# Performance work log

Hardware: AMD Instinct MI355X
Metric: run time of the kernel (lower is better)

The kernel has to match this reference:

```python
import jax, jax.numpy as jnp
import numpy as np

E = 512   # embed_dim
H = 16    # num_heads
D = E // H  # head_dim = 32
L = 2048  # target (query) length
S = 2048  # source (stored pattern) length
N = 4     # batch
LN_EPS = 1e-5


def setup_inputs() -> dict:
    key = jax.random.key(0)
    ks = jax.random.split(key, 8)
    inv_sqrt_e = 1.0 / np.sqrt(E).astype(np.float32)
    return {
        "query": jax.random.normal(ks[0], (L, N, E), jnp.float32),
        "key_in": jax.random.normal(ks[1], (S, N, E), jnp.float32),
        "value": jax.random.normal(ks[2], (S, N, E), jnp.float32),
        "scaling": jax.random.uniform(ks[3], (H,), jnp.float32),  # per-head beta
        "in_proj_weight": jax.random.normal(ks[4], (3 * E, E), jnp.float32) * inv_sqrt_e,
        "in_proj_bias": jnp.zeros((3 * E,), jnp.float32),
        "p_norm_weight": jnp.ones((D,), jnp.float32),
        "p_norm_bias": jnp.zeros((D,), jnp.float32),
        "out_proj_weight": jax.random.normal(ks[5], (E, E), jnp.float32) * inv_sqrt_e,
        "out_proj_bias": jnp.zeros((E,), jnp.float32),
    }


def reference(query, key_in, value, scaling, in_proj_weight, in_proj_bias,
              p_norm_weight, p_norm_bias, out_proj_weight, out_proj_bias):
    Lq, Nb, Ed = query.shape
    Sk = key_in.shape[0]
    # split packed in-projection (torch Linear convention: y = x @ W^T + b)
    wq, wk, wv = jnp.split(in_proj_weight, 3, axis=0)
    bq, bk, bv = jnp.split(in_proj_bias, 3, axis=0)
    q = jnp.einsum('lne,fe->lnf', query, wq) + bq
    k = jnp.einsum('sne,fe->snf', key_in, wk) + bk
    v = jnp.einsum('sne,fe->snf', value, wv) + bv
    # (len, N, H*D) -> (N, H, len, D)
    q = q.reshape(Lq, Nb, H, D).transpose(1, 2, 0, 3)
    k = k.reshape(Sk, Nb, H, D).transpose(1, 2, 0, 3)
    v = v.reshape(Sk, Nb, H, D).transpose(1, 2, 0, 3)

    def pattern_norm(x):
        # affine LayerNorm over the association (head) dimension D
        mu = jnp.mean(x, axis=-1, keepdims=True)
        var = jnp.mean(jnp.square(x - mu), axis=-1, keepdims=True)
        return (x - mu) * jax.lax.rsqrt(var + LN_EPS) * p_norm_weight + p_norm_bias

    k = pattern_norm(k)
    v = pattern_norm(v)

    beta = scaling.reshape(1, H, 1, 1)  # per-head inverse-temperature
    scores = jnp.einsum('nhld,nhsd->nhls', q * beta, k)  # [N,H,L,S]
    attn = jax.nn.softmax(scores, axis=-1)  # single Hopfield update (update_steps_max=0)
    out = jnp.einsum('nhls,nhsd->nhld', attn, v)  # [N,H,L,D]
    out = out.transpose(2, 0, 1, 3).reshape(Lq, Nb, H * D)
    out = jnp.einsum('lnf,of->lno', out, out_proj_weight) + out_proj_bias
    return out  # (L, N, E)
```

## Files before the change

kernel.cpp:

```cpp
#include <hip/hip_runtime.h>
#include <cstdint>

#define LN_EPS 1e-5f

typedef _Float16 f16;
typedef _Float16 half4_t __attribute__((ext_vector_type(4)));
typedef _Float16 half8_t __attribute__((ext_vector_type(8)));
typedef __fp16 fp16v2 __attribute__((ext_vector_type(2)));
typedef float f32x4 __attribute__((ext_vector_type(4)));

__device__ __forceinline__ void gl_lds16(const void* g, void* l) {
    __builtin_amdgcn_global_load_lds(
        (__attribute__((address_space(1))) void*)(uintptr_t)g,
        (__attribute__((address_space(3))) void*)(uint32_t)(uintptr_t)l,
        16, 0, 0);
}

__device__ __forceinline__ half4_t pack4(float a, float b, float c, float d) {
    fp16v2 lo = __builtin_amdgcn_cvt_pkrtz(a, b);
    fp16v2 hi = __builtin_amdgcn_cvt_pkrtz(c, d);
    half4_t r;
    r[0] = (f16)lo[0]; r[1] = (f16)lo[1]; r[2] = (f16)hi[0]; r[3] = (f16)hi[1];
    return r;
}

__global__ void k_cast(const float* __restrict__ W1f, const float* __restrict__ W2f,
                       const float* __restrict__ Xq, const float* __restrict__ Xk,
                       const float* __restrict__ Xv,
                       f16* __restrict__ W1h, f16* __restrict__ W2h,
                       f16* __restrict__ Xh) {
    int t0 = blockIdx.x * blockDim.x + threadIdx.x;
    #pragma unroll
    for (int rep = 0; rep < 4; ++rep) {
        int t = t0 + rep * 851968;
        const float4* src;
        half4_t* dst;
        int idx;
        if (t < 196608)      { src = (const float4*)W1f; dst = (half4_t*)W1h; idx = t; }
        else if (t < 262144) { src = (const float4*)W2f; dst = (half4_t*)W2h; idx = t - 196608; }
        else {
            int u = t - 262144;
            int s = u >> 20;
            idx = u & 1048575;
            src = (s == 0) ? (const float4*)Xq : ((s == 1) ? (const float4*)Xk : (const float4*)Xv);
            dst = (half4_t*)(Xh + (size_t)s * 4194304);
        }
        float4 v = src[idx];
        dst[idx] = pack4(v.x, v.y, v.z, v.w);
    }
}

__global__ __launch_bounds__(256) void k_inproj(
    const f16* __restrict__ Xh, const f16* __restrict__ W1,
    const float* __restrict__ bias, const float* __restrict__ scaling,
    const float* __restrict__ pnw, const float* __restrict__ pnb,
    f16* __restrict__ Qg, f16* __restrict__ Kg, f16* __restrict__ Vtg)
{
    __shared__ __align__(16) char pool[49152];

    const int tid = threadIdx.x;
    const int bid = blockIdx.x;
    const int jj = bid >> 3;
    const int m0 = ((bid & 7) * 8 + (jj & 7)) * 128;
    const int f0 = (jj >> 3) * 128;
    const int sec = f0 >> 9;
    const f16* X = Xh + (size_t)sec * 4194304;
    f16* Ob = (sec == 0) ? Qg : Kg;

    const int wid = tid >> 6, ln = tid & 63, l15 = ln & 15, quad = ln >> 4;
    const int wm = wid >> 1, wn = wid & 1;
    const int srow = ln >> 2, sco = (ln & 3) * 8;

    f32x4 z4 = {0.f, 0.f, 0.f, 0.f};
    f32x4 acc[4][4];
    #pragma unroll
    for (int i = 0; i < 4; ++i)
        #pragma unroll
        for (int j = 0; j < 4; ++j) acc[i][j] = z4;

    auto issue = [&](int kt, int slot) {
        const int k0 = kt * 32;
        f16* As = (f16*)(pool + slot * 16384);
        f16* Bs = (f16*)(pool + slot * 16384 + 8192);
        #pragma unroll
        for (int i = 0; i < 2; ++i) {
            int row = wid * 32 + i * 16 + srow;
            gl_lds16(W1 + (size_t)(f0 + row) * 512 + k0 + sco,
                     Bs + (wid * 32 + i * 16) * 32);
            gl_lds16(X + (size_t)(m0 + row) * 512 + k0 + sco,
                     As + (wid * 32 + i * 16) * 32);
        }
    };
    issue(0, 0);
    issue(1, 1);

    int slot = 0;
    for (int kt = 0; kt < 16; ++kt) {
        if (kt < 15) asm volatile("s_waitcnt vmcnt(4)" ::: "memory");
        else         asm volatile("s_waitcnt vmcnt(0)" ::: "memory");
        __builtin_amdgcn_s_barrier();

        if (kt < 14) {
            int nb = slot + 2; if (nb >= 3) nb -= 3;
            issue(kt + 2, nb);
        }

        const f16* As = (const f16*)(pool + slot * 16384);
        const f16* Bs = (const f16*)(pool + slot * 16384 + 8192);
        half8_t a[4], b[4];
        #pragma unroll
        for (int i = 0; i < 4; ++i)
            a[i] = *(const half8_t*)(As + (wm * 64 + i * 16 + l15) * 32 + quad * 8);
        #pragma unroll
        for (int j = 0; j < 4; ++j)
            b[j] = *(const half8_t*)(Bs + (wn * 64 + j * 16 + l15) * 32 + quad * 8);
        __builtin_amdgcn_s_setprio(1);
        #pragma unroll
        for (int i = 0; i < 4; ++i)
            #pragma unroll
            for (int j = 0; j < 4; ++j)
                acc[i][j] = __builtin_amdgcn_mfma_f32_16x16x32_f16(b[j], a[i], acc[i][j], 0, 0, 0);
        __builtin_amdgcn_s_setprio(0);

        slot = slot + 1; if (slot == 3) slot = 0;
    }

    __syncthreads();
    f16* Ep = (f16*)pool;

    float sA = 0.f, sB = 0.f;
    float4 wA, wB, bA, bB;
    if (sec == 0) {
        int hbase = ((f0 & 511) >> 5) + wn * 2;
        sA = scaling[hbase] * 1.44269504f;
        sB = scaling[hbase + 1] * 1.44269504f;
    } else {
        wA = *(const float4*)(pnw + quad * 4);
        wB = *(const float4*)(pnw + 16 + quad * 4);
        bA = *(const float4*)(pnb + quad * 4);
        bB = *(const float4*)(pnb + 16 + quad * 4);
    }
    float4 bias4[4];
    #pragma unroll
    for (int j = 0; j < 4; ++j)
        bias4[j] = *(const float4*)(bias + f0 + wn * 64 + j * 16 + quad * 4);

    #pragma unroll
    for (int i = 0; i < 4; ++i) {
        float x[4][4];
        #pragma unroll
        for (int j = 0; j < 4; ++j) {
            x[j][0] = acc[i][j][0] + bias4[j].x;
            x[j][1] = acc[i][j][1] + bias4[j].y;
            x[j][2] = acc[i][j][2] + bias4[j].z;
            x[j][3] = acc[i][j][3] + bias4[j].w;
        }
        if (sec == 0) {
            #pragma unroll
            for (int j = 0; j < 4; ++j) {
                float sc = (j < 2) ? sA : sB;
                #pragma unroll
                for (int r = 0; r < 4; ++r) x[j][r] *= sc;
            }
        } else {
            #pragma unroll
            for (int hp = 0; hp < 2; ++hp) {
                float s1 = 0.f, s2 = 0.f;
                #pragma unroll
                for (int jq = 0; jq < 2; ++jq) {
                    int j = hp * 2 + jq;
                    #pragma unroll
                    for (int r = 0; r < 4; ++r) { s1 += x[j][r]; s2 += x[j][r] * x[j][r]; }
                }
                s1 += __shfl_xor(s1, 16); s1 += __shfl_xor(s1, 32);
                s2 += __shfl_xor(s2, 16); s2 += __shfl_xor(s2, 32);
                float mu = s1 * (1.f / 32.f);
                float rs = rsqrtf(s2 * (1.f / 32.f) - mu * mu + LN_EPS);
                #pragma unroll
                for (int jq = 0; jq < 2; ++jq) {
                    int j = hp * 2 + jq;
                    const float4& wv = (j & 1) ? wB : wA;
                    const float4& bv = (j & 1) ? bB : bA;
                    x[j][0] = (x[j][0] - mu) * rs * wv.x + bv.x;
                    x[j][1] = (x[j][1] - mu) * rs * wv.y + bv.y;
                    x[j][2] = (x[j][2] - mu) * rs * wv.z + bv.z;
                    x[j][3] = (x[j][3] - mu) * rs * wv.w + bv.w;
                }
            }
        }
        int mloc = wm * 64 + i * 16 + l15;
        int key = (mloc >> 2) & 7;
        #pragma unroll
        for (int j = 0; j < 4; ++j) {
            int floc0 = wn * 64 + j * 16 + quad * 4;
            *(half4_t*)(Ep + mloc * 128 + (floc0 ^ (key << 3))) =
                pack4(x[j][0], x[j][1], x[j][2], x[j][3]);
        }
    }
    __syncthreads();

    if (sec < 2) {
        int fgrp = (tid >> 6) * 4 + quad;
        int fs = (f0 & 511) + fgrp * 8;
        int hh = fs >> 5, cc = (fs >> 3) & 3;
        #pragma unroll
        for (int it = 0; it < 8; ++it) {
            int nb = it & 3, lblk = it >> 2;
            int L = lblk * 16 + l15;
            int mloc = nb + 4 * L;
            half8_t v = *(const half8_t*)(Ep + mloc * 128 + ((fgrp ^ (L & 7)) << 3));
            int gg = nb * 16 + hh;
            size_t l = (size_t)(m0 >> 2) + L;
            *(half8_t*)(Ob + (size_t)gg * 65536 + (size_t)cc * 16384 + l * 8) = v;
        }
    } else {
        int seg = m0 >> 8;
        int csb = ((m0 >> 7) & 1) * 4;
        int hbase = (f0 & 511) >> 5;
        #pragma unroll
        for (int p = 0; p < 2; ++p) {
            int idx = tid * 2 + p;
            int g16 = idx >> 5, d = idx & 31;
            int nb = g16 >> 2, hhl = g16 & 3;
            int floc = hhl * 32 + d;
            size_t obase = (size_t)((nb * 16 + hbase + hhl) * 32 + seg) * 2048 + d * 64;
            #pragma unroll
            for (int cq = 0; cq < 4; ++cq) {
                half8_t hv;
                #pragma unroll
                for (int es = 0; es < 8; ++es) {
                    int mloc = nb + 4 * (cq * 8 + es);
                    hv[es] = Ep[mloc * 128 + (floc ^ (es << 3))];
                }
                int csx = (csb + cq) ^ (d & 7);
                *(half8_t*)(Vtg + obase + csx * 8) = hv;
            }
        }
    }
}

__global__ __launch_bounds__(256, 4) void k_flash(
    const f16* __restrict__ Qg, const f16* __restrict__ Kg,
    const f16* __restrict__ Vtg, f16* __restrict__ Og)
{
    __shared__ __align__(16) char smem[40960];

    const int tid = threadIdx.x, wid = tid >> 6, ln = tid & 63;
    const int l15 = ln & 15, quad = ln >> 4, l8 = ln & 7;
    char* Pw = smem + 24576 + wid * 4096;
    const int g = blockIdx.x, h = g & 15, n = g >> 4;
    const int q0 = blockIdx.y * 128;

    half8_t aq[2];
    #pragma unroll
    for (int i = 0; i < 2; ++i)
        aq[i] = *(const half8_t*)(Qg + (size_t)g * 65536 + (size_t)quad * 16384 +
                                  (size_t)(q0 + wid * 32 + i * 16 + l15) * 8);

    const f16* kp = Kg + (size_t)g * 65536 + (size_t)wid * 16384;
    const f16* vp = Vtg + (size_t)(g * 32) * 2048 + wid * 512;
    gl_lds16(kp + (size_t)ln * 8, smem + wid * 1024);
    gl_lds16(vp + (size_t)ln * 8, smem + 12288 + wid * 1024);
    gl_lds16(kp + 512 + (size_t)ln * 8, smem + 4096 + wid * 1024);
    gl_lds16(vp + 2048 + (size_t)ln * 8, smem + 12288 + 4096 + wid * 1024);
    kp += 1024;
    vp += 4096;

    half8_t onesf;
    {
        f16 o = (l15 == 0) ? (f16)1.0f : (f16)0.0f;
        #pragma unroll
        for (int j = 0; j < 8; ++j) onesf[j] = o;
    }

    f32x4 z4 = {0.f, 0.f, 0.f, 0.f};
    f32x4 accO[2][2], accSum[2];
    accO[0][0] = z4; accO[0][1] = z4; accO[1][0] = z4; accO[1][1] = z4;
    accSum[0] = z4; accSum[1] = z4;
    float m_i[2] = {-1e30f, -1e30f};

    const char* K0s = smem;          const char* V0s = smem + 12288;
    const char* K1s = smem + 4096;   const char* V1s = smem + 16384;
    const char* K2s = smem + 8192;   const char* V2s = smem + 20480;

    auto body = [&](const char* Kl, const char* Vt, char* Kn, char* Vn, int st) {
        if (st < 31) asm volatile("s_waitcnt vmcnt(2)" ::: "memory");
        else         asm volatile("s_waitcnt vmcnt(0)" ::: "memory");
        __builtin_amdgcn_s_barrier();

        if (st < 30) {
            gl_lds16(kp + (size_t)ln * 8, Kn + wid * 1024);
            gl_lds16(vp + (size_t)ln * 8, Vn + wid * 1024);
            kp += 512;
            vp += 2048;
        }

        half8_t ak[4];
        #pragma unroll
        for (int mt = 0; mt < 4; ++mt)
            ak[mt] = *(const half8_t*)(Kl + quad * 1024 + (mt * 16 + l15) * 16);
        f32x4 accS[2][4];
        __builtin_amdgcn_s_setprio(1);
        #pragma unroll
        for (int i = 0; i < 2; ++i)
            #pragma unroll
            for (int mt = 0; mt < 4; ++mt)
                accS[i][mt] = __builtin_amdgcn_mfma_f32_16x16x32_f16(ak[mt], aq[i], z4, 0, 0, 0);
        __builtin_amdgcn_s_setprio(0);

        float mn[2];
        bool up = false;
        #pragma unroll
        for (int i = 0; i < 2; ++i) {
            float xm = fmaxf(fmaxf(accS[i][0][0], accS[i][0][1]), accS[i][0][2]);
            xm = fmaxf(fmaxf(xm, accS[i][0][3]), accS[i][1][0]);
            xm = fmaxf(fmaxf(xm, accS[i][1][1]), accS[i][1][2]);
            xm = fmaxf(fmaxf(xm, accS[i][1][3]), accS[i][2][0]);
            xm = fmaxf(fmaxf(xm, accS[i][2][1]), accS[i][2][2]);
            xm = fmaxf(fmaxf(xm, accS[i][2][3]), accS[i][3][0]);
            xm = fmaxf(fmaxf(xm, accS[i][3][1]), accS[i][3][2]);
            xm = fmaxf(xm, accS[i][3][3]);
            xm = fmaxf(xm, __shfl_xor(xm, 16));
            xm = fmaxf(xm, __shfl_xor(xm, 32));
            up = up || (xm > m_i[i] + 8.f);
            mn[i] = fmaxf(m_i[i], xm);
        }
        if (__ballot(up)) {
            #pragma unroll
            for (int i = 0; i < 2; ++i) {
                float alpha = __builtin_amdgcn_exp2f(m_i[i] - mn[i]);
                #pragma unroll
                for (int dt = 0; dt < 2; ++dt)
                    #pragma unroll
                    for (int r = 0; r < 4; ++r) accO[i][dt][r] *= alpha;
                #pragma unroll
                for (int r = 0; r < 4; ++r) accSum[i][r] *= alpha;
                m_i[i] = mn[i];
            }
        }

        #pragma unroll
        for (int i = 0; i < 2; ++i) {
            #pragma unroll
            for (int mt = 0; mt < 4; ++mt) {
                float p0 = __builtin_amdgcn_exp2f(accS[i][mt][0] - m_i[i]);
                float p1 = __builtin_amdgcn_exp2f(accS[i][mt][1] - m_i[i]);
                float p2 = __builtin_amdgcn_exp2f(accS[i][mt][2] - m_i[i]);
                float p3 = __builtin_amdgcn_exp2f(accS[i][mt][3] - m_i[i]);
                int ch = (mt * 2 + (quad >> 1)) ^ l8;
                *(half4_t*)(Pw + (i * 16 + l15) * 128 + ch * 16 + (quad & 1) * 8) =
                    pack4(p0, p1, p2, p3);
            }
        }

        #pragma unroll
        for (int kt = 0; kt < 2; ++kt) {
            half8_t av[2], bp[2];
            #pragma unroll
            for (int dt = 0; dt < 2; ++dt) {
                int d = dt * 16 + l15;
                int cp = (kt * 4 + quad) ^ (l15 & 7);
                av[dt] = *(const half8_t*)(Vt + d * 128 + cp * 16);
            }
            #pragma unroll
            for (int i = 0; i < 2; ++i)
                bp[i] = *(const half8_t*)(Pw + (i * 16 + l15) * 128 +
                                          (((kt * 4 + quad) ^ l8) * 16));
            __builtin_amdgcn_s_setprio(1);
            #pragma unroll
            for (int i = 0; i < 2; ++i) {
                #pragma unroll
                for (int dt = 0; dt < 2; ++dt)
                    accO[i][dt] = __builtin_amdgcn_mfma_f32_16x16x32_f16(av[dt], bp[i], accO[i][dt], 0, 0, 0);
                accSum[i] = __builtin_amdgcn_mfma_f32_16x16x32_f16(onesf, bp[i], accSum[i], 0, 0, 0);
            }
            __builtin_amdgcn_s_setprio(0);
        }
    };

    #pragma unroll 1
    for (int tt = 0; tt < 10; ++tt) {
        body(K0s, V0s, (char*)K2s, (char*)V2s, tt * 3);
        body(K1s, V1s, (char*)K0s, (char*)V0s, tt * 3 + 1);
        body(K2s, V2s, (char*)K1s, (char*)V1s, tt * 3 + 2);
    }
    body(K0s, V0s, (char*)K2s, (char*)V2s, 30);
    body(K1s, V1s, (char*)K0s, (char*)V0s, 31);

    #pragma unroll
    for (int i = 0; i < 2; ++i) {
        float li = __shfl(accSum[i][0], l15);
        float inv = 1.f / li;
        #pragma unroll
        for (int dt = 0; dt < 2; ++dt)
            *(half4_t*)(Pw + (i * 16 + l15) * 80 + (dt * 16 + quad * 4) * 2) =
                pack4(accO[i][dt][0] * inv, accO[i][dt][1] * inv,
                      accO[i][dt][2] * inv, accO[i][dt][3] * inv);
    }
    int q2 = ln >> 1, hf = ln & 1;
    half8_t o0 = *(const half8_t*)(Pw + q2 * 80 + hf * 32);
    half8_t o1 = *(const half8_t*)(Pw + q2 * 80 + hf * 32 + 16);
    size_t rowe = ((size_t)(n * 2048 + q0 + wid * 32 + q2)) * 512 + h * 32 + hf * 16;
    *(half8_t*)(Og + rowe) = o0;
    *(half8_t*)(Og + rowe + 8) = o1;
}

__global__ __launch_bounds__(256) void k_outproj(
    const f16* __restrict__ A, const f16* __restrict__ W2,
    const float* __restrict__ bias, float* __restrict__ Out)
{
    __shared__ __align__(16) char pool[36864];

    const int tid = threadIdx.x;
    const int m0 = blockIdx.x * 64;
    const int f0 = blockIdx.y * 128;
    const int wid = tid >> 6, ln = tid & 63, l15 = ln & 15, quad = ln >> 4;
    const int wm = wid >> 1, wn = wid & 1;
    const int srow = ln >> 2, sco = (ln & 3) * 8;

    f32x4 z4 = {0.f, 0.f, 0.f, 0.f};
    f32x4 acc[2][4];
    #pragma unroll
    for (int i = 0; i < 2; ++i)
        #pragma unroll
        for (int j = 0; j < 4; ++j) acc[i][j] = z4;

    auto issue = [&](int kt, int slot) {
        const int k0 = kt * 32;
        f16* As = (f16*)(pool + slot * 12288);
        f16* Bs = (f16*)(pool + slot * 12288 + 4096);
        int arow = wid * 16 + srow;
        gl_lds16(A + (size_t)(m0 + arow) * 512 + k0 + sco,
                 As + wid * 512);
        #pragma unroll
        for (int i = 0; i < 2; ++i) {
            int brow = wid * 32 + i * 16 + srow;
            gl_lds16(W2 + (size_t)(f0 + brow) * 512 + k0 + sco,
                     Bs + (wid * 32 + i * 16) * 32);
        }
    };
    issue(0, 0);
    issue(1, 1);

    int slot = 0;
    for (int kt = 0; kt < 16; ++kt) {
        if (kt < 15) asm volatile("s_waitcnt vmcnt(3)" ::: "memory");
        else         asm volatile("s_waitcnt vmcnt(0)" ::: "memory");
        __builtin_amdgcn_s_barrier();

        if (kt < 14) {
            int nb = slot + 2; if (nb >= 3) nb -= 3;
            issue(kt + 2, nb);
        }

        const f16* As = (const f16*)(pool + slot * 12288);
        const f16* Bs = (const f16*)(pool + slot * 12288 + 4096);
        half8_t a[2], b[4];
        #pragma unroll
        for (int i = 0; i < 2; ++i)
            a[i] = *(const half8_t*)(As + (wm * 32 + i * 16 + l15) * 32 + quad * 8);
        #pragma unroll
        for (int j = 0; j < 4; ++j)
            b[j] = *(const half8_t*)(Bs + (wn * 64 + j * 16 + l15) * 32 + quad * 8);
        __builtin_amdgcn_s_setprio(1);
        #pragma unroll
        for (int i = 0; i < 2; ++i)
            #pragma unroll
            for (int j = 0; j < 4; ++j)
                acc[i][j] = __builtin_amdgcn_mfma_f32_16x16x32_f16(b[j], a[i], acc[i][j], 0, 0, 0);
        __builtin_amdgcn_s_setprio(0);

        slot = slot + 1; if (slot == 3) slot = 0;
    }

    __syncthreads();
    float* Ef = (float*)pool;

    #pragma unroll
    for (int j = 0; j < 4; ++j) {
        int floc0 = wn * 64 + j * 16 + quad * 4;
        float4 bs4 = *(const float4*)(bias + f0 + floc0);
        #pragma unroll
        for (int i = 0; i < 2; ++i) {
            int mloc = wm * 32 + i * 16 + l15;
            float4 o;
            o.x = acc[i][j][0] + bs4.x;
            o.y = acc[i][j][1] + bs4.y;
            o.z = acc[i][j][2] + bs4.z;
            o.w = acc[i][j][3] + bs4.w;
            *(float4*)(Ef + mloc * 132 + floc0) = o;
        }
    }
    __syncthreads();

    {
        int hw = tid >> 5, lane32 = tid & 31;
        #pragma unroll
        for (int it = 0; it < 8; ++it) {
            int row = it * 8 + hw;
            float4 v = *(const float4*)(Ef + row * 132 + lane32 * 4);
            int rm = m0 + row;
            int orow = (rm & 2047) * 4 + (rm >> 11);
            *(float4*)(Out + (size_t)orow * 512 + f0 + lane32 * 4) = v;
        }
    }
}

extern "C" void kernel_launch(void* const* d_in, const int* in_sizes, int n_in,
                              void* d_out, int out_size, void* d_ws, size_t ws_size,
                              hipStream_t stream) {
    const float* query   = (const float*)d_in[0];
    const float* key_in  = (const float*)d_in[1];
    const float* value   = (const float*)d_in[2];
    const float* scaling = (const float*)d_in[3];
    const float* ipw     = (const float*)d_in[4];
    const float* ipb     = (const float*)d_in[5];
    const float* pnw     = (const float*)d_in[6];
    const float* pnb     = (const float*)d_in[7];
    const float* opw     = (const float*)d_in[8];
    const float* opb     = (const float*)d_in[9];
    float* out = (float*)d_out;

    f16* Qg  = (f16*)d_ws;
    f16* Kg  = Qg + (size_t)4194304;
    f16* Vtg = Qg + (size_t)8388608;
    f16* W1  = Qg + (size_t)12582912;
    f16* W2  = Qg + (size_t)13369344;
    f16* Xh  = Qg + (size_t)13631488;
    f16* Og  = Xh;

    k_cast<<<3328, 256, 0, stream>>>(ipw, opw, query, key_in, value, W1, W2, Xh);
    k_inproj<<<768, 256, 0, stream>>>(Xh, W1, ipb, scaling, pnw, pnb, Qg, Kg, Vtg);
    k_flash<<<dim3(64, 16), 256, 0, stream>>>(Qg, Kg, Vtg, Og);
    k_outproj<<<dim3(128, 4), 256, 0, stream>>>(Og, W2, opb, out);
}
```

Baseline: 205.5 us.

## Fuse activation fp32-to-fp16 cast into in-projection GEMM A-tile loads

Removes the separate cast of query/key/value to fp16. The in-projection kernel now reads fp32 activations into registers, converts them, and writes them to LDS, while the weights still go through direct global-to-LDS loads. The three-stage LDS ring becomes a two-stage double buffer with register prefetch two k-steps ahead. This avoids writing and re-reading about 50 MB of fp16 intermediates, at the cost of doubled global read bytes for the A tiles, more VGPRs, and an extra LDS wait each iteration.

```diff
diff --git a/kernel.cpp b/kernel.cpp
--- a/kernel.cpp
+++ b/kernel.cpp
@@ -25,38 +25,25 @@
 }
 
 __global__ void k_cast(const float* __restrict__ W1f, const float* __restrict__ W2f,
-                       const float* __restrict__ Xq, const float* __restrict__ Xk,
-                       const float* __restrict__ Xv,
-                       f16* __restrict__ W1h, f16* __restrict__ W2h,
-                       f16* __restrict__ Xh) {
-    int t0 = blockIdx.x * blockDim.x + threadIdx.x;
-    #pragma unroll
-    for (int rep = 0; rep < 4; ++rep) {
-        int t = t0 + rep * 851968;
-        const float4* src;
-        half4_t* dst;
-        int idx;
-        if (t < 196608)      { src = (const float4*)W1f; dst = (half4_t*)W1h; idx = t; }
-        else if (t < 262144) { src = (const float4*)W2f; dst = (half4_t*)W2h; idx = t - 196608; }
-        else {
-            int u = t - 262144;
-            int s = u >> 20;
-            idx = u & 1048575;
-            src = (s == 0) ? (const float4*)Xq : ((s == 1) ? (const float4*)Xk : (const float4*)Xv);
-            dst = (half4_t*)(Xh + (size_t)s * 4194304);
-        }
-        float4 v = src[idx];
-        dst[idx] = pack4(v.x, v.y, v.z, v.w);
-    }
+                       f16* __restrict__ W1h, f16* __restrict__ W2h) {
+    int t = blockIdx.x * blockDim.x + threadIdx.x;
+    const float4* src;
+    half4_t* dst;
+    int idx;
+    if (t < 196608) { src = (const float4*)W1f; dst = (half4_t*)W1h; idx = t; }
+    else            { src = (const float4*)W2f; dst = (half4_t*)W2h; idx = t - 196608; }
+    float4 v = src[idx];
+    dst[idx] = pack4(v.x, v.y, v.z, v.w);
 }
 
 __global__ __launch_bounds__(256) void k_inproj(
-    const f16* __restrict__ Xh, const f16* __restrict__ W1,
+    const float* __restrict__ Xq, const float* __restrict__ Xk,
+    const float* __restrict__ Xv, const f16* __restrict__ W1,
     const float* __restrict__ bias, const float* __restrict__ scaling,
     const float* __restrict__ pnw, const float* __restrict__ pnb,
     f16* __restrict__ Qg, f16* __restrict__ Kg, f16* __restrict__ Vtg)
 {
-    __shared__ __align__(16) char pool[49152];
+    __shared__ __align__(16) char pool[32768];
 
     const int tid = threadIdx.x;
     const int bid = blockIdx.x;
@@ -64,13 +51,21 @@
     const int m0 = ((bid & 7) * 8 + (jj & 7)) * 128;
     const int f0 = (jj >> 3) * 128;
     const int sec = f0 >> 9;
-    const f16* X = Xh + (size_t)sec * 4194304;
+    const float* X = (sec == 0) ? Xq : ((sec == 1) ? Xk : Xv);
     f16* Ob = (sec == 0) ? Qg : Kg;
 
     const int wid = tid >> 6, ln = tid & 63, l15 = ln & 15, quad = ln >> 4;
     const int wm = wid >> 1, wn = wid & 1;
     const int srow = ln >> 2, sco = (ln & 3) * 8;
 
+    f16* B0s = (f16*)(pool);
+    f16* B1s = (f16*)(pool + 8192);
+    f16* A0s = (f16*)(pool + 16384);
+    f16* A1s = (f16*)(pool + 24576);
+
+    const float* Xr0 = X + (size_t)(m0 + wid * 32 + srow) * 512 + sco;
+    const float* Xr1 = Xr0 + 16 * 512;
+
     f32x4 z4 = {0.f, 0.f, 0.f, 0.f};
     f32x4 acc[4][4];
     #pragma unroll
@@ -78,42 +73,65 @@
         #pragma unroll
         for (int j = 0; j < 4; ++j) acc[i][j] = z4;
 
-    auto issue = [&](int kt, int slot) {
+    auto issueB = [&](int kt, f16* Bs) {
         const int k0 = kt * 32;
-        f16* As = (f16*)(pool + slot * 16384);
-        f16* Bs = (f16*)(pool + slot * 16384 + 8192);
         #pragma unroll
         for (int i = 0; i < 2; ++i) {
             int row = wid * 32 + i * 16 + srow;
             gl_lds16(W1 + (size_t)(f0 + row) * 512 + k0 + sco,
                      Bs + (wid * 32 + i * 16) * 32);
-            gl_lds16(X + (size_t)(m0 + row) * 512 + k0 + sco,
-                     As + (wid * 32 + i * 16) * 32);
         }
     };
-    issue(0, 0);
-    issue(1, 1);
-
-    int slot = 0;
-    for (int kt = 0; kt < 16; ++kt) {
+    auto writeA = [&](f16* As, const float4& r0, const float4& r1,
+                      const float4& r2, const float4& r3) {
+        half4_t lo = pack4(r0.x, r0.y, r0.z, r0.w);
+        half4_t hi = pack4(r1.x, r1.y, r1.z, r1.w);
+        half8_t h;
+        h[0] = lo[0]; h[1] = lo[1]; h[2] = lo[2]; h[3] = lo[3];
+        h[4] = hi[0]; h[5] = hi[1]; h[6] = hi[2]; h[7] = hi[3];
+        *(half8_t*)(As + (wid * 32 + srow) * 32 + sco) = h;
+        lo = pack4(r2.x, r2.y, r2.z, r2.w);
+        hi = pack4(r3.x, r3.y, r3.z, r3.w);
+        h[0] = lo[0]; h[1] = lo[1]; h[2] = lo[2]; h[3] = lo[3];
+        h[4] = hi[0]; h[5] = hi[1]; h[6] = hi[2]; h[7] = hi[3];
+        *(half8_t*)(As + (wid * 32 + 16 + srow) * 32 + sco) = h;
+    };
+
+    float4 sA0, sA1, sA2, sA3;
+    float4 sB0, sB1, sB2, sB3;
+
+    sA0 = *(const float4*)(Xr0);      sA1 = *(const float4*)(Xr0 + 4);
+    sA2 = *(const float4*)(Xr1);      sA3 = *(const float4*)(Xr1 + 4);
+    issueB(0, B0s);
+    writeA(A0s, sA0, sA1, sA2, sA3);
+    sB0 = *(const float4*)(Xr0 + 32); sB1 = *(const float4*)(Xr0 + 36);
+    sB2 = *(const float4*)(Xr1 + 32); sB3 = *(const float4*)(Xr1 + 36);
+
+    auto body = [&](int kt, const f16* AsR, const f16* BsR, f16* BsW, f16* AsW,
+                    float4& w0, float4& w1, float4& w2, float4& w3,
+                    float4& d0, float4& d1, float4& d2, float4& d3) {
         if (kt < 15) asm volatile("s_waitcnt vmcnt(4)" ::: "memory");
         else         asm volatile("s_waitcnt vmcnt(0)" ::: "memory");
+        asm volatile("s_waitcnt lgkmcnt(0)" ::: "memory");
         __builtin_amdgcn_s_barrier();
 
+        if (kt < 15) issueB(kt + 1, BsW);
         if (kt < 14) {
-            int nb = slot + 2; if (nb >= 3) nb -= 3;
-            issue(kt + 2, nb);
-        }
-
-        const f16* As = (const f16*)(pool + slot * 16384);
-        const f16* Bs = (const f16*)(pool + slot * 16384 + 8192);
+            const int k2 = (kt + 2) * 32;
+            d0 = *(const float4*)(Xr0 + k2);
+            d1 = *(const float4*)(Xr0 + k2 + 4);
+            d2 = *(const float4*)(Xr1 + k2);
+            d3 = *(const float4*)(Xr1 + k2 + 4);
+        }
+        if (kt < 15) writeA(AsW, w0, w1, w2, w3);
+
         half8_t a[4], b[4];
         #pragma unroll
         for (int i = 0; i < 4; ++i)
-            a[i] = *(const half8_t*)(As + (wm * 64 + i * 16 + l15) * 32 + quad * 8);
+            a[i] = *(const half8_t*)(AsR + (wm * 64 + i * 16 + l15) * 32 + quad * 8);
         #pragma unroll
         for (int j = 0; j < 4; ++j)
-            b[j] = *(const half8_t*)(Bs + (wn * 64 + j * 16 + l15) * 32 + quad * 8);
+            b[j] = *(const half8_t*)(BsR + (wn * 64 + j * 16 + l15) * 32 + quad * 8);
         __builtin_amdgcn_s_setprio(1);
         #pragma unroll
         for (int i = 0; i < 4; ++i)
@@ -121,19 +139,24 @@
             for (int j = 0; j < 4; ++j)
                 acc[i][j] = __builtin_amdgcn_mfma_f32_16x16x32_f16(b[j], a[i], acc[i][j], 0, 0, 0);
         __builtin_amdgcn_s_setprio(0);
-
-        slot = slot + 1; if (slot == 3) slot = 0;
+    };
+
+    #pragma unroll 1
+    for (int tt = 0; tt < 8; ++tt) {
+        int kt = tt * 2;
+        body(kt,     A0s, B0s, B1s, A1s, sB0, sB1, sB2, sB3, sA0, sA1, sA2, sA3);
+        body(kt + 1, A1s, B1s, B0s, A0s, sA0, sA1, sA2, sA3, sB0, sB1, sB2, sB3);
     }
 
     __syncthreads();
     f16* Ep = (f16*)pool;
 
-    float sA = 0.f, sB = 0.f;
+    float sQa = 0.f, sQb = 0.f;
     float4 wA, wB, bA, bB;
     if (sec == 0) {
         int hbase = ((f0 & 511) >> 5) + wn * 2;
-        sA = scaling[hbase] * 1.44269504f;
-        sB = scaling[hbase + 1] * 1.44269504f;
+        sQa = scaling[hbase] * 1.44269504f;
+        sQb = scaling[hbase + 1] * 1.44269504f;
     } else {
         wA = *(const float4*)(pnw + quad * 4);
         wB = *(const float4*)(pnw + 16 + quad * 4);
@@ -158,7 +181,7 @@
         if (sec == 0) {
             #pragma unroll
             for (int j = 0; j < 4; ++j) {
-                float sc = (j < 2) ? sA : sB;
+                float sc = (j < 2) ? sQa : sQb;
                 #pragma unroll
                 for (int r = 0; r < 4; ++r) x[j][r] *= sc;
             }
@@ -526,11 +549,10 @@
     f16* Vtg = Qg + (size_t)8388608;
     f16* W1  = Qg + (size_t)12582912;
     f16* W2  = Qg + (size_t)13369344;
-    f16* Xh  = Qg + (size_t)13631488;
-    f16* Og  = Xh;
-
-    k_cast<<<3328, 256, 0, stream>>>(ipw, opw, query, key_in, value, W1, W2, Xh);
-    k_inproj<<<768, 256, 0, stream>>>(Xh, W1, ipb, scaling, pnw, pnb, Qg, Kg, Vtg);
+    f16* Og  = Qg + (size_t)13631488;
+
+    k_cast<<<1024, 256, 0, stream>>>(ipw, opw, W1, W2);
+    k_inproj<<<768, 256, 0, stream>>>(query, key_in, value, W1, ipb, scaling, pnw, pnb, Qg, Kg, Vtg);
     k_flash<<<dim3(64, 16), 256, 0, stream>>>(Qg, Kg, Vtg, Og);
     k_outproj<<<dim3(128, 4), 256, 0, stream>>>(Og, W2, opb, out);
 }
```

Result: slower. 214.3 us (+4.3%).
